# Kernel tuning notes

Measured on AMD Instinct MI355X. Metric: run time of the kernel, lower is better.

Reference implementation:

```python
import math
import jax, jax.numpy as jnp
import numpy as np

IN_SIZE = 1024
OUT_SIZE = 1024
LOG_N = 10          # ceil(log2(in_size))
NSTACKS = 1         # ceil(out_size / 2**LOG_N)
NBLOCKS = 1


def setup_inputs() -> dict:
    key = jax.random.key(0)
    k1, k2, k3 = jax.random.split(key, 3)
    x = jax.random.normal(k1, (8, 4096, IN_SIZE), dtype=jnp.float32)
    # twiddle init: randn * 1/sqrt(2)  (ortho_init=False, real)
    twiddle = jax.random.normal(
        k2, (NSTACKS, NBLOCKS, LOG_N, IN_SIZE // 2, 2, 2), dtype=jnp.float32
    ) * (1.0 / math.sqrt(2.0))
    bound = 1.0 / math.sqrt(IN_SIZE)
    bias = jax.random.uniform(k3, (OUT_SIZE,), minval=-bound, maxval=bound,
                              dtype=jnp.float32)
    return {"x": x, "twiddle": twiddle, "bias": bias}


def butterfly_multiply(twiddle, x, increasing_stride=True):
    """twiddle: (nstacks, nblocks, log_n, n/2, 2, 2); x: (batch, nstacks, n)."""
    b, nstacks, n = x.shape
    nblocks, log_n = twiddle.shape[1], twiddle.shape[2]
    out = x
    inc = increasing_stride
    for blk in range(nblocks):
        for idx in range(log_n):
            log_stride = idx if inc else log_n - 1 - idx
            stride = 1 << log_stride
            # t: (nstacks, n/(2*stride), stride, 2, 2)
            t = twiddle[:, blk, idx].reshape(nstacks, n // (2 * stride), stride, 2, 2)
            # o: (batch, nstacks, n/(2*stride), 2, stride)
            o = out.reshape(b, nstacks, n // (2 * stride), 2, stride)
            # 2x2 rotation applied across pairs separated by `stride`
            out = jnp.einsum('sgrij,bsgjr->bsgir', t, o).reshape(b, nstacks, n)
        inc = not inc
    return out


def reference(x, twiddle, bias):
    batch_shape = x.shape[:-1]
    xf = x.reshape(-1, IN_SIZE)                       # pre_process (no pad: 1024=2**10)
    xb = jnp.broadcast_to(xf[:, None, :], (xf.shape[0], NSTACKS, IN_SIZE))
    out = butterfly_multiply(twiddle, xb, increasing_stride=True)
    out = out.reshape(xf.shape[0], NSTACKS * IN_SIZE)[:, :OUT_SIZE]
    out = out + bias
    return out.reshape(*batch_shape, OUT_SIZE)
```

## Files before the change

### kernel.cpp

```cpp
#include <hip/hip_runtime.h>


#define N 1024
#define BLOCK_THREADS 512
#define WAVES_PER_BLOCK 8
#define ROWS_PER_WAVE 4
#define NSTAGES 10

__global__ __launch_bounds__(256) void permute_tw_kernel(
    const float* __restrict__ tw, float* __restrict__ ws)
{
    const int s = blockIdx.x;
    const int t = threadIdx.x;
    #pragma unroll
    for (int it = 0; it < 8; ++it) {
        const int g = it * 256 + t;
        const float val = tw[s * 2048 + g];
        int dst;
        if (s < 4) {
            const int l  = g >> 5;
            const int r  = g & 31;
            dst = (r >> 2) * 256 + l * 4 + (r & 3);
        } else {
            const int p  = g >> 2;
            const int c  = g & 3;
            const int i  = c >> 1;
            const int j  = c & 1;
            const int pl = p >> 4;
            const int k  = p & 15;
            const int lm = s - 4;
            const int m  = 1 << lm;
            const int l  = ((pl >> lm) << (lm + 1)) | (i << lm) | (pl & (m - 1));
            dst = (k >> 1) * 256 + l * 4 + (k & 1) * 2 + (j ^ i);
        }
        ws[s * 2048 + dst] = val;
    }
}

template<int M>
__device__ __forceinline__ float sx(float v) {
    if constexpr (M < 32) {
        return __int_as_float(__builtin_amdgcn_ds_swizzle(
            __float_as_int(v), (M << 10) | 0x1f));
    } else {
        return __shfl_xor(v, 32, 64);
    }
}

__global__ __launch_bounds__(BLOCK_THREADS) void butterfly_kernel(
    const float* __restrict__ x,
    const float* __restrict__ ws,
    const float* __restrict__ bias,
    float* __restrict__ out,
    int nRows)
{
    extern __shared__ float ldsTw[];

    {
        const int t = threadIdx.x;
        const float4* src = (const float4*)ws;
        float4* dst = (float4*)ldsTw;
        #pragma unroll
        for (int i = 0; i < (NSTAGES * 2048 / 4) / BLOCK_THREADS; ++i)
            dst[i * BLOCK_THREADS + t] = src[i * BLOCK_THREADS + t];
    }
    __syncthreads();

    const int lane = threadIdx.x & 63;
    const int off = lane * 16;
    const int waveId = blockIdx.x * WAVES_PER_BLOCK + (threadIdx.x >> 6);
    const long rowBase = (long)waveId * ROWS_PER_WAVE;
    if (rowBase >= nRows) return;

    float v[ROWS_PER_WAVE][16];

    #pragma unroll
    for (int r = 0; r < ROWS_PER_WAVE; ++r) {
        const float4* p = (const float4*)(x + (rowBase + r) * N + off);
        #pragma unroll
        for (int q = 0; q < 4; ++q) {
            float4 f = p[q];
            v[r][q*4+0] = f.x; v[r][q*4+1] = f.y;
            v[r][q*4+2] = f.z; v[r][q*4+3] = f.w;
        }
    }

    #pragma unroll
    for (int stage = 0; stage < 4; ++stage) {
        const int s = 1 << stage;
        float t[32];
        const float4* tp = (const float4*)(ldsTw + stage * 2048) + lane;
        #pragma unroll
        for (int q = 0; q < 8; ++q) {
            float4 f = tp[q * 64];
            t[q*4+0] = f.x; t[q*4+1] = f.y; t[q*4+2] = f.z; t[q*4+3] = f.w;
        }
        #pragma unroll
        for (int r = 0; r < ROWS_PER_WAVE; ++r) {
            #pragma unroll
            for (int j = 0; j < 8; ++j) {
                const int p0 = ((j >> stage) << (stage + 1)) | (j & (s - 1));
                const int p1 = p0 | s;
                float a = v[r][p0], b = v[r][p1];
                v[r][p0] = t[j*4+0] * a + t[j*4+1] * b;
                v[r][p1] = t[j*4+2] * a + t[j*4+3] * b;
            }
        }
    }

#define XSTAGE(STG) { \
    constexpr int M = 1 << ((STG) - 4); \
    float ta_[16], tb_[16]; \
    const float4* tp = (const float4*)(ldsTw + (STG) * 2048) + lane; \
    _Pragma("unroll") \
    for (int kk = 0; kk < 8; ++kk) { \
        float4 f = tp[kk * 64]; \
        ta_[2*kk+0] = f.x; tb_[2*kk+0] = f.y; \
        ta_[2*kk+1] = f.z; tb_[2*kk+1] = f.w; } \
    _Pragma("unroll") \
    for (int r = 0; r < ROWS_PER_WAVE; ++r) { \
        _Pragma("unroll") \
        for (int k = 0; k < 16; ++k) { \
            float mine  = v[r][k]; \
            float other = sx<M>(mine); \
            v[r][k] = ta_[k] * mine + tb_[k] * other; } } \
}
    XSTAGE(4)
    XSTAGE(5)
    XSTAGE(6)
    XSTAGE(7)
    XSTAGE(8)
    XSTAGE(9)
#undef XSTAGE

    float bv[16];
    {
        const float4* bp = (const float4*)(bias + off);
        #pragma unroll
        for (int q = 0; q < 4; ++q) {
            float4 f = bp[q];
            bv[q*4+0] = f.x; bv[q*4+1] = f.y;
            bv[q*4+2] = f.z; bv[q*4+3] = f.w;
        }
    }
    #pragma unroll
    for (int r = 0; r < ROWS_PER_WAVE; ++r) {
        float4* p = (float4*)(out + (rowBase + r) * N + off);
        #pragma unroll
        for (int q = 0; q < 4; ++q) {
            float4 f;
            f.x = v[r][q*4+0] + bv[q*4+0];
            f.y = v[r][q*4+1] + bv[q*4+1];
            f.z = v[r][q*4+2] + bv[q*4+2];
            f.w = v[r][q*4+3] + bv[q*4+3];
            p[q] = f;
        }
    }
}

extern "C" void kernel_launch(void* const* d_in, const int* in_sizes, int n_in,
                              void* d_out, int out_size, void* d_ws, size_t ws_size,
                              hipStream_t stream) {
    const float* x    = (const float*)d_in[0];
    const float* tw   = (const float*)d_in[1];
    const float* bias = (const float*)d_in[2];
    float* out = (float*)d_out;
    float* ws  = (float*)d_ws;

    const size_t ldsBytes = (size_t)NSTAGES * 2048 * sizeof(float);
    static bool attrSet = false;
    if (!attrSet) {
        hipFuncSetAttribute((const void*)butterfly_kernel,
                            hipFuncAttributeMaxDynamicSharedMemorySize,
                            (int)ldsBytes);
        attrSet = true;
    }

    permute_tw_kernel<<<10, 256, 0, stream>>>(tw, ws);

    const int nRows = in_sizes[0] / N;
    const int rowsPerBlock = WAVES_PER_BLOCK * ROWS_PER_WAVE;
    const int blocks = (nRows + rowsPerBlock - 1) / rowsPerBlock;

    butterfly_kernel<<<blocks, BLOCK_THREADS, ldsBytes, stream>>>(
        x, ws, bias, out, nRows);
}
```

Baseline: 267.3 us.

## Transpose rows via LDS mid-pipeline to make late butterfly stages thread-local

Stages 4-5 now use DPP quad permutes instead of ds_swizzle. Each wave then transposes its rows through a per-wave LDS buffer so that stages 6-9 become in-register butterflies, removing cross-lane shuffles for the largest strides. Stage 6-9 twiddles are read directly from the raw global twiddle tensor, and stage 4-5 twiddles from the permuted global workspace. Output is written strided per lane instead of with float4 stores. The LDS footprint grows with the transpose buffers, and the stores are no longer vectorised.

```diff
diff --git a/kernel.cpp b/kernel.cpp
--- a/kernel.cpp
+++ b/kernel.cpp
@@ -5,7 +5,9 @@
 #define BLOCK_THREADS 512
 #define WAVES_PER_BLOCK 8
 #define ROWS_PER_WAVE 4
-#define NSTAGES 10
+#define TBUF_FLOATS 1280
+#define LDS_TW_FLOATS 8192
+#define LDS_TOTAL_FLOATS (LDS_TW_FLOATS + WAVES_PER_BLOCK * TBUF_FLOATS)
 
 __global__ __launch_bounds__(256) void permute_tw_kernel(
     const float* __restrict__ tw, float* __restrict__ ws)
@@ -37,41 +39,41 @@
     }
 }
 
-template<int M>
-__device__ __forceinline__ float sx(float v) {
-    if constexpr (M < 32) {
-        return __int_as_float(__builtin_amdgcn_ds_swizzle(
-            __float_as_int(v), (M << 10) | 0x1f));
-    } else {
-        return __shfl_xor(v, 32, 64);
-    }
+template<int CTRL>
+__device__ __forceinline__ float qperm(float v) {
+    return __int_as_float(__builtin_amdgcn_mov_dpp(
+        __float_as_int(v), CTRL, 0xF, 0xF, true));
 }
 
 __global__ __launch_bounds__(BLOCK_THREADS) void butterfly_kernel(
     const float* __restrict__ x,
+    const float* __restrict__ tw,
     const float* __restrict__ ws,
     const float* __restrict__ bias,
     float* __restrict__ out,
     int nRows)
 {
-    extern __shared__ float ldsTw[];
+    extern __shared__ float lds[];
 
     {
         const int t = threadIdx.x;
         const float4* src = (const float4*)ws;
-        float4* dst = (float4*)ldsTw;
-        #pragma unroll
-        for (int i = 0; i < (NSTAGES * 2048 / 4) / BLOCK_THREADS; ++i)
+        float4* dst = (float4*)lds;
+        #pragma unroll
+        for (int i = 0; i < (LDS_TW_FLOATS / 4) / BLOCK_THREADS; ++i)
             dst[i * BLOCK_THREADS + t] = src[i * BLOCK_THREADS + t];
     }
     __syncthreads();
 
     const int lane = threadIdx.x & 63;
-    const int off = lane * 16;
-    const int waveId = blockIdx.x * WAVES_PER_BLOCK + (threadIdx.x >> 6);
+    const int wib  = threadIdx.x >> 6;
+    float* tbuf = lds + LDS_TW_FLOATS + wib * TBUF_FLOATS;
+
+    const int waveId = blockIdx.x * WAVES_PER_BLOCK + wib;
     const long rowBase = (long)waveId * ROWS_PER_WAVE;
     if (rowBase >= nRows) return;
 
+    const int off = lane * 16;
     float v[ROWS_PER_WAVE][16];
 
     #pragma unroll
@@ -89,7 +91,7 @@
     for (int stage = 0; stage < 4; ++stage) {
         const int s = 1 << stage;
         float t[32];
-        const float4* tp = (const float4*)(ldsTw + stage * 2048) + lane;
+        const float4* tp = (const float4*)(lds + stage * 2048) + lane;
         #pragma unroll
         for (int q = 0; q < 8; ++q) {
             float4 f = tp[q * 64];
@@ -108,13 +110,12 @@
         }
     }
 
-#define XSTAGE(STG) { \
-    constexpr int M = 1 << ((STG) - 4); \
+#define DSTAGE(STG, CTRL) { \
     float ta_[16], tb_[16]; \
-    const float4* tp = (const float4*)(ldsTw + (STG) * 2048) + lane; \
+    const float4* tp = (const float4*)(ws + (STG) * 2048) + lane; \
     _Pragma("unroll") \
     for (int kk = 0; kk < 8; ++kk) { \
-        float4 f = tp[kk * 64]; \
+        float4 f = tp[kk * 64];             \
         ta_[2*kk+0] = f.x; tb_[2*kk+0] = f.y; \
         ta_[2*kk+1] = f.z; tb_[2*kk+1] = f.w; } \
     _Pragma("unroll") \
@@ -122,39 +123,67 @@
         _Pragma("unroll") \
         for (int k = 0; k < 16; ++k) { \
             float mine  = v[r][k]; \
-            float other = sx<M>(mine); \
+            float other = qperm<CTRL>(mine); \
             v[r][k] = ta_[k] * mine + tb_[k] * other; } } \
 }
-    XSTAGE(4)
-    XSTAGE(5)
-    XSTAGE(6)
-    XSTAGE(7)
-    XSTAGE(8)
-    XSTAGE(9)
-#undef XSTAGE
+    DSTAGE(4, 0xB1)
+    DSTAGE(5, 0x4E)
+#undef DSTAGE
+
+    {
+        float4* tb4 = (float4*)tbuf;
+        const int rbase = (lane >> 4) * 20 + (lane & 15);
+        #pragma unroll
+        for (int r = 0; r < ROWS_PER_WAVE; ++r) {
+            #pragma unroll
+            for (int k = 0; k < 4; ++k) {
+                float4 f;
+                f.x = v[r][4*k+0]; f.y = v[r][4*k+1];
+                f.z = v[r][4*k+2]; f.w = v[r][4*k+3];
+                tb4[lane * 5 + k] = f;
+            }
+            #pragma unroll
+            for (int j = 0; j < 16; ++j)
+                v[r][j] = tbuf[rbase + j * 80];
+        }
+    }
+
+    #pragma unroll
+    for (int m = 0; m < 4; ++m) {
+        const int s = 1 << m;
+        float t[32];
+        const float4* tp = (const float4*)(tw + (6 + m) * 2048) + lane;
+        #pragma unroll
+        for (int q = 0; q < 8; ++q) {
+            float4 f = tp[q * 64];
+            t[q*4+0] = f.x; t[q*4+1] = f.y; t[q*4+2] = f.z; t[q*4+3] = f.w;
+        }
+        #pragma unroll
+        for (int r = 0; r < ROWS_PER_WAVE; ++r) {
+            #pragma unroll
+            for (int j = 0; j < 8; ++j) {
+                const int p0 = ((j >> m) << (m + 1)) | (j & (s - 1));
+                const int p1 = p0 | s;
+                float a = v[r][p0], b = v[r][p1];
+                v[r][p0] = t[j*4+0] * a + t[j*4+1] * b;
+                v[r][p1] = t[j*4+2] * a + t[j*4+3] * b;
+            }
+        }
+    }
 
     float bv[16];
     {
-        const float4* bp = (const float4*)(bias + off);
-        #pragma unroll
-        for (int q = 0; q < 4; ++q) {
-            float4 f = bp[q];
-            bv[q*4+0] = f.x; bv[q*4+1] = f.y;
-            bv[q*4+2] = f.z; bv[q*4+3] = f.w;
-        }
+        const float* bp = bias + lane;
+        #pragma unroll
+        for (int j = 0; j < 16; ++j)
+            bv[j] = bp[j * 64];
     }
     #pragma unroll
     for (int r = 0; r < ROWS_PER_WAVE; ++r) {
-        float4* p = (float4*)(out + (rowBase + r) * N + off);
-        #pragma unroll
-        for (int q = 0; q < 4; ++q) {
-            float4 f;
-            f.x = v[r][q*4+0] + bv[q*4+0];
-            f.y = v[r][q*4+1] + bv[q*4+1];
-            f.z = v[r][q*4+2] + bv[q*4+2];
-            f.w = v[r][q*4+3] + bv[q*4+3];
-            p[q] = f;
-        }
+        float* op = out + (rowBase + r) * N + lane;
+        #pragma unroll
+        for (int j = 0; j < 16; ++j)
+            op[j * 64] = v[r][j] + bv[j];
     }
 }
 
@@ -167,7 +196,7 @@
     float* out = (float*)d_out;
     float* ws  = (float*)d_ws;
 
-    const size_t ldsBytes = (size_t)NSTAGES * 2048 * sizeof(float);
+    const size_t ldsBytes = (size_t)LDS_TOTAL_FLOATS * sizeof(float);
     static bool attrSet = false;
     if (!attrSet) {
         hipFuncSetAttribute((const void*)butterfly_kernel,
@@ -183,5 +212,5 @@
     const int blocks = (nRows + rowsPerBlock - 1) / rowsPerBlock;
 
     butterfly_kernel<<<blocks, BLOCK_THREADS, ldsBytes, stream>>>(
-        x, ws, bias, out, nRows);
-}
+        x, tw, ws, bias, out, nRows);
+}
```

New measurement: 255.1 us. 1.05x faster.
